# Performance work log

Hardware: AMD Instinct MI355X
Metric: run time of the kernel (lower is better)

## Reference

```python
import jax, jax.numpy as jnp
import numpy as np

NOPE, ROPE, VDIM, QKD = 128, 64, 128, 192
H = 16
EPS = 1e-6
SCALING = QKD ** -0.5


def rms_norm(x, w):
    xf = x.astype(jnp.float32)
    var = jnp.mean(xf * xf, axis=-1, keepdims=True)
    return (w * (xf * jax.lax.rsqrt(var + EPS))).astype(x.dtype)


def rotate_half(x):
    d = x.shape[-1] // 2
    return jnp.concatenate((-x[..., d:], x[..., :d]), axis=-1)


def apply_rope(q, k, cos, sin):
    # cos/sin: [B,S,D] -> unsqueeze head dim
    cos = cos[:, None, :, :]
    sin = sin[:, None, :, :]
    return q * cos + rotate_half(q) * sin, k * cos + rotate_half(k) * sin


def setup_inputs() -> dict:
    key = jax.random.key(0)
    ks = jax.random.split(key, 8)
    B, S, D = 2, 2048, 2048
    pos = jnp.arange(S, dtype=jnp.float32)
    inv_freq = 1.0 / (10000.0 ** (jnp.arange(0, ROPE, 2, dtype=jnp.float32) / ROPE))
    ang = pos[:, None] * inv_freq[None, :]            # [S, ROPE/2]
    emb = jnp.concatenate([ang, ang], axis=-1)        # [S, ROPE]
    cos = jnp.broadcast_to(jnp.cos(emb)[None], (B, S, ROPE))
    sin = jnp.broadcast_to(jnp.sin(emb)[None], (B, S, ROPE))
    s = lambda k, shp, fan: jax.random.normal(k, shp, jnp.float32) * (fan ** -0.5)
    return {
        "hidden_states": jax.random.normal(ks[0], (B, S, D), jnp.float32),
        "cos": cos,
        "sin": sin,
        "q_a_W": s(ks[1], (1536, D), D),
        "q_a_norm_w": jnp.ones((1536,), jnp.float32),
        "q_b_W": s(ks[2], (H * QKD, 1536), 1536),
        "kv_a_W": s(ks[3], (512 + ROPE, D), D),
        "kv_a_norm_w": jnp.ones((512,), jnp.float32),
        "kv_b_W": s(ks[4], (H * (NOPE + VDIM), 512), 512),
        "o_W": s(ks[5], (D, H * VDIM), H * VDIM),
    }


def reference(hidden_states, cos, sin, q_a_W, q_a_norm_w, q_b_W, kv_a_W,
              kv_a_norm_w, kv_b_W, o_W):
    B, S, D = hidden_states.shape
    # low-rank Q path
    q = rms_norm(hidden_states @ q_a_W.T, q_a_norm_w) @ q_b_W.T   # [B,S,H*QKD]
    q = q.reshape(B, S, H, QKD).transpose(0, 2, 1, 3)             # [B,H,S,QKD]
    q_pass, q_rot = q[..., :NOPE], q[..., NOPE:]
    # compressed KV path
    ckv = hidden_states @ kv_a_W.T                                # [B,S,512+ROPE]
    k_lat, k_rot = ckv[..., :512], ckv[..., 512:]
    kv = rms_norm(k_lat, kv_a_norm_w) @ kv_b_W.T                  # [B,S,H*(NOPE+VDIM)]
    kv = kv.reshape(B, S, H, NOPE + VDIM).transpose(0, 2, 1, 3)   # [B,H,S,*]
    k_pass, v = kv[..., :NOPE], kv[..., NOPE:]
    k_rot = k_rot.reshape(B, 1, S, ROPE)
    q_rot, k_rot = apply_rope(q_rot, k_rot, cos, sin)
    k_rot = jnp.broadcast_to(k_rot, (B, H, S, ROPE))
    query = jnp.concatenate((q_pass, q_rot), axis=-1)             # [B,H,S,QKD]
    key = jnp.concatenate((k_pass, k_rot), axis=-1)
    # eager causal attention
    scores = jnp.einsum('bhsd,bhtd->bhst', query, key) * SCALING
    causal = jnp.tril(jnp.ones((S, S), bool))
    scores = jnp.where(causal, scores, jnp.finfo(scores.dtype).min)
    attn = jax.nn.softmax(scores.astype(jnp.float32), axis=-1).astype(query.dtype)
    out = jnp.einsum('bhst,bhtd->bhsd', attn, v)                  # [B,H,S,VDIM]
    out = out.transpose(0, 2, 1, 3).reshape(B, S, H * VDIM)
    return out @ o_W.T
```

## Files before the change

### kernel.cpp

```cpp
#include <hip/hip_runtime.h>
#include <hip/hip_bf16.h>


typedef __bf16 bf16x8 __attribute__((ext_vector_type(8)));
typedef float floatx4 __attribute__((ext_vector_type(4)));
#define BF16 __hip_bfloat16

static __device__ __forceinline__ BF16 f2b(float x) { return __float2bfloat16(x); }
static __device__ __forceinline__ unsigned short b2u(BF16 x) { return *(unsigned short*)&x; }
static __device__ __forceinline__ float fast_exp2(float x) { return __builtin_amdgcn_exp2f(x); }

static __device__ __forceinline__ void load_lds16(const BF16* g, BF16* l) {
  __builtin_amdgcn_global_load_lds((__attribute__((address_space(1))) void*)(void*)g,
                                   (__attribute__((address_space(3))) void*)(void*)l,
                                   16, 0, 0);
}

struct CastArgs {
  const float* src[6];
  BF16* dst[6];
  long n[6];
};
__global__ void cast_multi_k(CastArgs a) {
  int r = blockIdx.y;
  long n = a.n[r];
  const float* __restrict__ x = a.src[r];
  BF16* __restrict__ y = a.dst[r];
  for (long i = ((long)blockIdx.x * 256 + threadIdx.x) * 4; i + 3 < n;
       i += (long)gridDim.x * 1024) {
    float4 v = *(const float4*)(x + i);
    y[i+0] = f2b(v.x); y[i+1] = f2b(v.y); y[i+2] = f2b(v.z); y[i+3] = f2b(v.w);
  }
}

template<int OUT_MODE>
__global__ __launch_bounds__(256) void gemm_lds(const BF16* __restrict__ A, const BF16* __restrict__ B,
                                                void* __restrict__ C, int M, int N, int K,
                                                const float* __restrict__ cosb,
                                                const float* __restrict__ sinb,
                                                BF16* __restrict__ P1, BF16* __restrict__ P2) {
  __shared__ __align__(16) BF16 As[128*32];
  __shared__ __align__(16) BF16 Bs[128*32];
  int tid = threadIdx.x, wave = tid >> 6, lane = tid & 63;
  int wr = wave >> 1, wc = wave & 1, lr = lane & 15, quad = lane >> 4;
  long m0 = (long)blockIdx.y * 128, n0 = (long)blockIdx.x * 128;

  int c0 = wave*64 + lane, c1 = c0 + 256;
  const BF16* ga0 = A + (m0 + (c0>>2))*(long)K + (c0&3)*8;
  const BF16* ga1 = A + (m0 + (c1>>2))*(long)K + (c1&3)*8;
  long bn0 = n0 + (c0>>2); if (bn0 >= N) bn0 = N-1;
  long bn1 = n0 + (c1>>2); if (bn1 >= N) bn1 = N-1;
  const BF16* gb0 = B + bn0*(long)K + (c0&3)*8;
  const BF16* gb1 = B + bn1*(long)K + (c1&3)*8;
  BF16* la0 = As + wave*512;
  BF16* la1 = As + wave*512 + 2048;
  BF16* lb0 = Bs + wave*512;
  BF16* lb1 = Bs + wave*512 + 2048;

  floatx4 acc[4][4] = {};
  for (int k0 = 0; k0 < K; k0 += 32) {
    __syncthreads();
    load_lds16(ga0 + k0, la0);
    load_lds16(ga1 + k0, la1);
    load_lds16(gb0 + k0, lb0);
    load_lds16(gb1 + k0, lb1);
    __syncthreads();
    bf16x8 a[4], b[4];
#pragma unroll
    for (int i = 0; i < 4; i++) a[i] = *(const bf16x8*)(As + (wr*64 + i*16 + lr)*32 + quad*8);
#pragma unroll
    for (int j = 0; j < 4; j++) b[j] = *(const bf16x8*)(Bs + (wc*64 + j*16 + lr)*32 + quad*8);
#pragma unroll
    for (int i = 0; i < 4; i++)
#pragma unroll
      for (int j = 0; j < 4; j++)
        acc[i][j] = __builtin_amdgcn_mfma_f32_16x16x32_bf16(a[i], b[j], acc[i][j], 0, 0, 0);
  }

  long n0w = n0 + wc*64;
  const float SCALE_L2E = 0.104117546f;
#pragma unroll
  for (int i = 0; i < 4; i++) {
    long tok = m0 + wr*64 + i*16 + quad*4;
    long bb = tok >> 11, s = tok & 2047;
    if (OUT_MODE == 0) {
#pragma unroll
      for (int r = 0; r < 4; r++) {
        long row = tok + r;
#pragma unroll
        for (int j = 0; j < 4; j++) {
          long col = n0w + j*16 + lr;
          if (col < N) ((float*)C)[row*(long)N + col] = acc[i][j][r];
        }
      }
    } else if (OUT_MODE == 2) {
#pragma unroll
      for (int j = 0; j < 4; j++) {
        long col = n0w + j*16 + lr;
        long h = col >> 8, d = col & 255;
        if (d < 128) {
#pragma unroll
          for (int r = 0; r < 4; r++)
            P1[((bb*16 + h)*2048 + s + r)*192 + d] = f2b(acc[i][j][r]);
        } else {
          ushort4 pk;
          pk.x = b2u(f2b(acc[i][j][0])); pk.y = b2u(f2b(acc[i][j][1]));
          pk.z = b2u(f2b(acc[i][j][2])); pk.w = b2u(f2b(acc[i][j][3]));
          *(ushort4*)(P2 + ((bb*16 + h)*128 + d - 128)*2048 + s) = pk;
        }
      }
    } else {
      bool rope = ((n0w % 192) == 128);
#pragma unroll
      for (int r = 0; r < 4; r++) {
        long row = tok + r;
#pragma unroll
        for (int j = 0; j < 4; j++) {
          long col = n0w + j*16 + lr;
          float x = acc[i][j][r], val;
          if (rope) {
            int id = j*16 + lr;
            float partner = acc[i][j^2][r];
            float rot = (j < 2) ? -partner : partner;
            val = x*cosb[row*64 + id] + rot*sinb[row*64 + id];
          } else {
            val = x;
          }
          long h = col / 192, d = col % 192;
          P1[((bb*16 + h)*2048 + s + r)*192 + d] = f2b(val * SCALE_L2E);
        }
      }
    }
  }
}

template<int D>
__global__ __launch_bounds__(256) void rmsnorm_k(const float* __restrict__ x, const float* __restrict__ w,
                                                 BF16* __restrict__ y, int ld_in, int ld_out) {
  long row = blockIdx.x;
  const float* xr = x + row * (long)ld_in;
  float ss = 0.f;
  for (int i = threadIdx.x * 4; i < D; i += 1024) {
    float4 v = *(const float4*)(xr + i);
    ss += v.x*v.x + v.y*v.y + v.z*v.z + v.w*v.w;
  }
#pragma unroll
  for (int off = 32; off > 0; off >>= 1) ss += __shfl_down(ss, off);
  __shared__ float red[4];
  if ((threadIdx.x & 63) == 0) red[threadIdx.x >> 6] = ss;
  __syncthreads();
  float tot = red[0] + red[1] + red[2] + red[3];
  float rs = rsqrtf(tot / (float)D + 1e-6f);
  BF16* yr = y + row * (long)ld_out;
  for (int i = threadIdx.x * 4; i < D; i += 1024) {
    float4 v = *(const float4*)(xr + i);
    yr[i+0] = f2b(v.x * w[i+0] * rs);
    yr[i+1] = f2b(v.y * w[i+1] * rs);
    yr[i+2] = f2b(v.z * w[i+2] * rs);
    yr[i+3] = f2b(v.w * w[i+3] * rs);
  }
}

__global__ void prep_krot_k(const float* __restrict__ krot, int ld, const float* __restrict__ cosb,
                            const float* __restrict__ sinb, BF16* __restrict__ Kt) {
  long row = blockIdx.x; int i = threadIdx.x;
  const float* kr = krot + row * (long)ld;
  float x = kr[i];
  float rot = (i < 32) ? -kr[i + 32] : kr[i - 32];
  BF16 v = f2b(x * cosb[row*64 + i] + rot * sinb[row*64 + i]);
  long b = row >> 11, s = row & 2047;
  long base = ((b*16)*2048 + s)*192 + 128 + i;
#pragma unroll
  for (int h = 0; h < 16; h++) Kt[base + (long)h*2048*192] = v;
}

#define LK 200
#define LV 72
#define LP 72
__global__ __launch_bounds__(256) void flash_k(const BF16* __restrict__ Qt, const BF16* __restrict__ Kt,
                                               const BF16* __restrict__ Vt, BF16* __restrict__ O) {
  __shared__ __align__(16) BF16 Ks[64*LK];
  __shared__ __align__(16) BF16 Vs[128*LV];
  __shared__ __align__(16) BF16 Ps[4][16*LP];
  int tid = threadIdx.x, wave = tid >> 6, lane = tid & 63;
  int lr = lane & 15, quad = lane >> 4;
  int F = blockIdx.x;
  int g = F & 31, jidx = F >> 5;
  int h = g & 15, b = g >> 4;
  const BF16* Qb = Qt + ((long)(b*16 + h) * 2048) * 192;
  const BF16* Kb = Kt + ((long)(b*16 + h) * 2048) * 192;
  const BF16* Vb = Vt + ((long)(b*16 + h) * 128) * 2048;
  const float NEG_INF = -__builtin_inff();

  int krow[6], kcol[6];
#pragma unroll
  for (int i = 0; i < 6; i++) {
    int c = tid + 256*i;
    krow[i] = c / 24; kcol[i] = (c % 24) * 8;
  }
  int vrow[4], vcol[4];
#pragma unroll
  for (int i = 0; i < 4; i++) {
    int c = tid + 256*i;
    vrow[i] = c >> 3; vcol[i] = (c & 7) * 8;
  }

  bf16x8 kreg[6], vreg[4];
  auto stage_load = [&](int k0) {
#pragma unroll
    for (int i = 0; i < 6; i++)
      kreg[i] = *(const bf16x8*)(Kb + (long)(k0 + krow[i])*192 + kcol[i]);
#pragma unroll
    for (int i = 0; i < 4; i++)
      vreg[i] = *(const bf16x8*)(Vb + (long)vrow[i]*2048 + k0 + vcol[i]);
  };
  auto stage_store = [&]() {
#pragma unroll
    for (int i = 0; i < 6; i++)
      *(bf16x8*)(Ks + krow[i]*LK + kcol[i]) = kreg[i];
#pragma unroll
    for (int i = 0; i < 4; i++)
      *(bf16x8*)(Vs + vrow[i]*LV + vcol[i]) = vreg[i];
  };

  for (int half = 0; half < 2; half++) {
    int qt = (half == 0) ? jidx : 31 - jidx;
    int q0 = qt * 64;
    bf16x8 qf[6];
    {
      const BF16* qp = Qb + (long)(q0 + wave*16 + lr) * 192 + quad*8;
#pragma unroll
      for (int f = 0; f < 6; f++) qf[f] = *(const bf16x8*)(qp + f*32);
    }
    float m_i[4], l_i[4];
#pragma unroll
    for (int r = 0; r < 4; r++) { m_i[r] = NEG_INF; l_i[r] = 0.f; }
    floatx4 o_acc[8] = {};
    int nk = qt + 1;
    stage_load(0);
    for (int kt = 0; kt < nk; kt++) {
      __syncthreads();
      stage_store();
      __syncthreads();
      if (kt + 1 < nk) stage_load((kt + 1) * 64);
      floatx4 st[4];
#pragma unroll
      for (int t = 0; t < 4; t++) {
        floatx4 c = {};
#pragma unroll
        for (int f = 0; f < 6; f++) {
          bf16x8 kf = *(const bf16x8*)(Ks + (t*16+lr)*LK + f*32 + quad*8);
          c = __builtin_amdgcn_mfma_f32_16x16x32_bf16(qf[f], kf, c, 0, 0, 0);
        }
        st[t] = c;
      }
      float mt[4];
#pragma unroll
      for (int r = 0; r < 4; r++) mt[r] = NEG_INF;
      if (kt == qt) {
#pragma unroll
        for (int t = 0; t < 4; t++) {
          int coff = t*16 + lr;
#pragma unroll
          for (int r = 0; r < 4; r++) {
            float sc = st[t][r];
            if (coff > wave*16 + quad*4 + r) sc = NEG_INF;
            st[t][r] = sc;
            mt[r] = fmaxf(mt[r], sc);
          }
        }
      } else {
#pragma unroll
        for (int t = 0; t < 4; t++)
#pragma unroll
          for (int r = 0; r < 4; r++) mt[r] = fmaxf(mt[r], st[t][r]);
      }
#pragma unroll
      for (int off = 1; off < 16; off <<= 1)
#pragma unroll
        for (int r = 0; r < 4; r++) mt[r] = fmaxf(mt[r], __shfl_xor(mt[r], off));
      float alpha[4], rsum[4];
#pragma unroll
      for (int r = 0; r < 4; r++) {
        float mn = fmaxf(m_i[r], mt[r]);
        alpha[r] = fast_exp2(m_i[r] - mn);
        m_i[r] = mn;
        rsum[r] = 0.f;
      }
#pragma unroll
      for (int t = 0; t < 4; t++)
#pragma unroll
        for (int r = 0; r < 4; r++) {
          float p = fast_exp2(st[t][r] - m_i[r]);
          st[t][r] = p;
          rsum[r] += p;
        }
#pragma unroll
      for (int off = 1; off < 16; off <<= 1)
#pragma unroll
        for (int r = 0; r < 4; r++) rsum[r] += __shfl_xor(rsum[r], off);
#pragma unroll
      for (int r = 0; r < 4; r++) l_i[r] = l_i[r]*alpha[r] + rsum[r];
#pragma unroll
      for (int v = 0; v < 8; v++)
#pragma unroll
        for (int r = 0; r < 4; r++) o_acc[v][r] *= alpha[r];
#pragma unroll
      for (int t = 0; t < 4; t++)
#pragma unroll
        for (int r = 0; r < 4; r++)
          Ps[wave][(quad*4 + r)*LP + t*16 + lr] = f2b(st[t][r]);
#pragma unroll
      for (int kc = 0; kc < 2; kc++) {
        bf16x8 pa = *(const bf16x8*)(&Ps[wave][lr*LP + kc*32 + quad*8]);
#pragma unroll
        for (int v = 0; v < 8; v++) {
          bf16x8 vf = *(const bf16x8*)(&Vs[(v*16+lr)*LV + kc*32 + quad*8]);
          o_acc[v] = __builtin_amdgcn_mfma_f32_16x16x32_bf16(pa, vf, o_acc[v], 0, 0, 0);
        }
      }
    }
    long rowb = q0 + wave*16 + quad*4;
#pragma unroll
    for (int v = 0; v < 8; v++)
#pragma unroll
      for (int r = 0; r < 4; r++) {
        long row = rowb + r;
        O[((long)b*2048 + row)*2048 + h*128 + v*16 + lr] = f2b(o_acc[v][r] / l_i[r]);
      }
  }
}

extern "C" void kernel_launch(void* const* d_in, const int* in_sizes, int n_in,
                              void* d_out, int out_size, void* d_ws, size_t ws_size,
                              hipStream_t stream) {
  const float* hidden      = (const float*)d_in[0];
  const float* cosb        = (const float*)d_in[1];
  const float* sinb        = (const float*)d_in[2];
  const float* q_a_W       = (const float*)d_in[3];
  const float* q_a_norm_w  = (const float*)d_in[4];
  const float* q_b_W       = (const float*)d_in[5];
  const float* kv_a_W      = (const float*)d_in[6];
  const float* kv_a_norm_w = (const float*)d_in[7];
  const float* kv_b_W      = (const float*)d_in[8];
  const float* o_W         = (const float*)d_in[9];
  float* out = (float*)d_out;

  const int Mrows = 4096;

  char* ws = (char*)d_ws; size_t off = 0;
  auto alloc = [&](size_t bytes) -> void* {
    void* p = ws + off; off = (off + bytes + 255) & ~(size_t)255; return p;
  };
  BF16* hb    = (BF16*)alloc((size_t)4096*2048*2);
  BF16* Wqakv = (BF16*)alloc((size_t)2112*2048*2);
  BF16* Wqb   = (BF16*)alloc((size_t)3072*1536*2);
  BF16* Wkvb  = (BF16*)alloc((size_t)4096*512*2);
  BF16* Wo    = (BF16*)alloc((size_t)2048*2048*2);
  float* qakv = (float*)alloc((size_t)4096*2112*4);
  BF16* qan   = (BF16*)alloc((size_t)4096*1536*2);
  BF16* kvn   = (BF16*)alloc((size_t)4096*512*2);
  BF16* Qt    = (BF16*)alloc((size_t)2*16*2048*192*2);
  BF16* Kt    = (BF16*)alloc((size_t)2*16*2048*192*2);
  BF16* Vt    = (BF16*)alloc((size_t)2*16*128*2048*2);
  BF16* attn  = (BF16*)alloc((size_t)4096*2048*2);

  CastArgs ca;
  ca.src[0] = hidden;  ca.dst[0] = hb;                 ca.n[0] = (long)4096*2048;
  ca.src[1] = q_a_W;   ca.dst[1] = Wqakv;              ca.n[1] = (long)1536*2048;
  ca.src[2] = kv_a_W;  ca.dst[2] = Wqakv + (long)1536*2048; ca.n[2] = (long)576*2048;
  ca.src[3] = q_b_W;   ca.dst[3] = Wqb;                ca.n[3] = (long)3072*1536;
  ca.src[4] = kv_b_W;  ca.dst[4] = Wkvb;               ca.n[4] = (long)4096*512;
  ca.src[5] = o_W;     ca.dst[5] = Wo;                 ca.n[5] = (long)2048*2048;
  cast_multi_k<<<dim3(1024, 6), dim3(256), 0, stream>>>(ca);

  gemm_lds<0><<<dim3(17, 32), dim3(256), 0, stream>>>(hb, Wqakv, qakv, Mrows, 2112, 2048,
                                                      nullptr, nullptr, nullptr, nullptr);
  rmsnorm_k<1536><<<dim3(4096), dim3(256), 0, stream>>>(qakv, q_a_norm_w, qan, 2112, 1536);
  rmsnorm_k<512><<<dim3(4096), dim3(256), 0, stream>>>(qakv + 1536, kv_a_norm_w, kvn, 2112, 512);
  prep_krot_k<<<dim3(4096), dim3(64), 0, stream>>>(qakv + 2048, 2112, cosb, sinb, Kt);

  gemm_lds<3><<<dim3(24, 32), dim3(256), 0, stream>>>(qan, Wqb, nullptr, Mrows, 3072, 1536,
                                                      cosb, sinb, Qt, nullptr);
  gemm_lds<2><<<dim3(32, 32), dim3(256), 0, stream>>>(kvn, Wkvb, nullptr, Mrows, 4096, 512,
                                                      nullptr, nullptr, Kt, Vt);

  flash_k<<<dim3(512), dim3(256), 0, stream>>>(Qt, Kt, Vt, attn);

  gemm_lds<0><<<dim3(16, 32), dim3(256), 0, stream>>>(attn, Wo, out, Mrows, 2048, 2048,
                                                      nullptr, nullptr, nullptr, nullptr);
}
```

Before: 490.4 us.

## Merge norm/rope kernels, batch Q and KV GEMMs, widen flash tiles

The two RMSNorm launches and the k_rot RoPE kernel become one per-row kernel. The Q-projection and KV-projection GEMMs run as a single launch split by block index. The flash attention kernel now uses 512-thread blocks over 128-row query tiles, so each K/V tile loaded into LDS is shared by 8 waves, with per-wave causal skipping. This cuts launch count and K/V global traffic, at the cost of half as many flash blocks and possible wave idling on diagonal tiles.

Measured after the change: 492.5 us. No clear change (+0.4%).

```diff
diff --git a/kernel.cpp b/kernel.cpp
--- a/kernel.cpp
+++ b/kernel.cpp
@@ -34,16 +34,13 @@
 }
 
 template<int OUT_MODE>
-__global__ __launch_bounds__(256) void gemm_lds(const BF16* __restrict__ A, const BF16* __restrict__ B,
-                                                void* __restrict__ C, int M, int N, int K,
-                                                const float* __restrict__ cosb,
-                                                const float* __restrict__ sinb,
-                                                BF16* __restrict__ P1, BF16* __restrict__ P2) {
-  __shared__ __align__(16) BF16 As[128*32];
-  __shared__ __align__(16) BF16 Bs[128*32];
+static __device__ __forceinline__ void gemm_body(
+    const BF16* __restrict__ A, const BF16* __restrict__ B, void* __restrict__ C,
+    int M, int N, int K, const float* __restrict__ cosb, const float* __restrict__ sinb,
+    BF16* __restrict__ P1, BF16* __restrict__ P2, int bx, int by, BF16* As, BF16* Bs) {
   int tid = threadIdx.x, wave = tid >> 6, lane = tid & 63;
   int wr = wave >> 1, wc = wave & 1, lr = lane & 15, quad = lane >> 4;
-  long m0 = (long)blockIdx.y * 128, n0 = (long)blockIdx.x * 128;
+  long m0 = (long)by * 128, n0 = (long)bx * 128;
 
   int c0 = wave*64 + lane, c1 = c0 + 256;
   const BF16* ga0 = A + (m0 + (c0>>2))*(long)K + (c0&3)*8;
@@ -134,101 +131,151 @@
   }
 }
 
-template<int D>
-__global__ __launch_bounds__(256) void rmsnorm_k(const float* __restrict__ x, const float* __restrict__ w,
-                                                 BF16* __restrict__ y, int ld_in, int ld_out) {
+__global__ __launch_bounds__(256) void gemm0_k(const BF16* __restrict__ A, const BF16* __restrict__ B,
+                                               float* __restrict__ C, int M, int N, int K) {
+  __shared__ __align__(16) BF16 As[128*32];
+  __shared__ __align__(16) BF16 Bs[128*32];
+  gemm_body<0>(A, B, C, M, N, K, nullptr, nullptr, nullptr, nullptr,
+               blockIdx.x, blockIdx.y, As, Bs);
+}
+
+__global__ __launch_bounds__(256) void gemm_qkv_k(const BF16* __restrict__ qan, const BF16* __restrict__ Wqb,
+                                                  const BF16* __restrict__ kvn, const BF16* __restrict__ Wkvb,
+                                                  const float* __restrict__ cosb, const float* __restrict__ sinb,
+                                                  BF16* __restrict__ Qt, BF16* __restrict__ Kt,
+                                                  BF16* __restrict__ Vt) {
+  __shared__ __align__(16) BF16 As[128*32];
+  __shared__ __align__(16) BF16 Bs[128*32];
+  int bid = blockIdx.x;
+  if (bid < 768) {
+    gemm_body<3>(qan, Wqb, nullptr, 4096, 3072, 1536, cosb, sinb, Qt, nullptr,
+                 bid % 24, bid / 24, As, Bs);
+  } else {
+    bid -= 768;
+    gemm_body<2>(kvn, Wkvb, nullptr, 4096, 4096, 512, nullptr, nullptr, Kt, Vt,
+                 bid % 32, bid / 32, As, Bs);
+  }
+}
+
+__global__ __launch_bounds__(256) void norms_k(const float* __restrict__ qakv,
+                                               const float* __restrict__ qw, const float* __restrict__ kw,
+                                               const float* __restrict__ cosb, const float* __restrict__ sinb,
+                                               BF16* __restrict__ qan, BF16* __restrict__ kvn,
+                                               BF16* __restrict__ Kt) {
   long row = blockIdx.x;
-  const float* xr = x + row * (long)ld_in;
-  float ss = 0.f;
-  for (int i = threadIdx.x * 4; i < D; i += 1024) {
-    float4 v = *(const float4*)(xr + i);
-    ss += v.x*v.x + v.y*v.y + v.z*v.z + v.w*v.w;
-  }
-#pragma unroll
-  for (int off = 32; off > 0; off >>= 1) ss += __shfl_down(ss, off);
+  const float* xr = qakv + row * 2112;
+  int tid = threadIdx.x;
   __shared__ float red[4];
-  if ((threadIdx.x & 63) == 0) red[threadIdx.x >> 6] = ss;
+  {
+    float ss = 0.f;
+    for (int i = tid*4; i < 1536; i += 1024) {
+      float4 v = *(const float4*)(xr + i);
+      ss += v.x*v.x + v.y*v.y + v.z*v.z + v.w*v.w;
+    }
+#pragma unroll
+    for (int off = 32; off > 0; off >>= 1) ss += __shfl_down(ss, off);
+    if ((tid & 63) == 0) red[tid >> 6] = ss;
+    __syncthreads();
+    float rs = rsqrtf((red[0]+red[1]+red[2]+red[3]) / 1536.f + 1e-6f);
+    BF16* yr = qan + row * 1536;
+    for (int i = tid*4; i < 1536; i += 1024) {
+      float4 v = *(const float4*)(xr + i);
+      yr[i+0] = f2b(v.x * qw[i+0] * rs);
+      yr[i+1] = f2b(v.y * qw[i+1] * rs);
+      yr[i+2] = f2b(v.z * qw[i+2] * rs);
+      yr[i+3] = f2b(v.w * qw[i+3] * rs);
+    }
+  }
   __syncthreads();
-  float tot = red[0] + red[1] + red[2] + red[3];
-  float rs = rsqrtf(tot / (float)D + 1e-6f);
-  BF16* yr = y + row * (long)ld_out;
-  for (int i = threadIdx.x * 4; i < D; i += 1024) {
-    float4 v = *(const float4*)(xr + i);
-    yr[i+0] = f2b(v.x * w[i+0] * rs);
-    yr[i+1] = f2b(v.y * w[i+1] * rs);
-    yr[i+2] = f2b(v.z * w[i+2] * rs);
-    yr[i+3] = f2b(v.w * w[i+3] * rs);
-  }
-}
-
-__global__ void prep_krot_k(const float* __restrict__ krot, int ld, const float* __restrict__ cosb,
-                            const float* __restrict__ sinb, BF16* __restrict__ Kt) {
-  long row = blockIdx.x; int i = threadIdx.x;
-  const float* kr = krot + row * (long)ld;
-  float x = kr[i];
-  float rot = (i < 32) ? -kr[i + 32] : kr[i - 32];
-  BF16 v = f2b(x * cosb[row*64 + i] + rot * sinb[row*64 + i]);
-  long b = row >> 11, s = row & 2047;
-  long base = ((b*16)*2048 + s)*192 + 128 + i;
-#pragma unroll
-  for (int h = 0; h < 16; h++) Kt[base + (long)h*2048*192] = v;
+  {
+    float ss = 0.f;
+    for (int i = tid*4; i < 512; i += 1024) {
+      float4 v = *(const float4*)(xr + 1536 + i);
+      ss += v.x*v.x + v.y*v.y + v.z*v.z + v.w*v.w;
+    }
+#pragma unroll
+    for (int off = 32; off > 0; off >>= 1) ss += __shfl_down(ss, off);
+    if ((tid & 63) == 0) red[tid >> 6] = ss;
+    __syncthreads();
+    float rs = rsqrtf((red[0]+red[1]+red[2]+red[3]) / 512.f + 1e-6f);
+    BF16* yr = kvn + row * 512;
+    for (int i = tid*4; i < 512; i += 1024) {
+      float4 v = *(const float4*)(xr + 1536 + i);
+      yr[i+0] = f2b(v.x * kw[i+0] * rs);
+      yr[i+1] = f2b(v.y * kw[i+1] * rs);
+      yr[i+2] = f2b(v.z * kw[i+2] * rs);
+      yr[i+3] = f2b(v.w * kw[i+3] * rs);
+    }
+  }
+  if (tid < 64) {
+    int i = tid;
+    const float* kr = xr + 2048;
+    float x = kr[i];
+    float rot = (i < 32) ? -kr[i + 32] : kr[i - 32];
+    BF16 v = f2b(x * cosb[row*64 + i] + rot * sinb[row*64 + i]);
+    long b = row >> 11, s = row & 2047;
+    long base = ((b*16)*2048 + s)*192 + 128 + i;
+#pragma unroll
+    for (int h = 0; h < 16; h++) Kt[base + (long)h*2048*192] = v;
+  }
 }
 
 #define LK 200
 #define LV 72
 #define LP 72
-__global__ __launch_bounds__(256) void flash_k(const BF16* __restrict__ Qt, const BF16* __restrict__ Kt,
+__global__ __launch_bounds__(512) void flash_k(const BF16* __restrict__ Qt, const BF16* __restrict__ Kt,
                                                const BF16* __restrict__ Vt, BF16* __restrict__ O) {
   __shared__ __align__(16) BF16 Ks[64*LK];
   __shared__ __align__(16) BF16 Vs[128*LV];
-  __shared__ __align__(16) BF16 Ps[4][16*LP];
+  __shared__ __align__(16) BF16 Ps[8][16*LP];
   int tid = threadIdx.x, wave = tid >> 6, lane = tid & 63;
   int lr = lane & 15, quad = lane >> 4;
   int F = blockIdx.x;
-  int g = F & 31, jidx = F >> 5;
+  int g = F & 31, j = F >> 5;
   int h = g & 15, b = g >> 4;
   const BF16* Qb = Qt + ((long)(b*16 + h) * 2048) * 192;
   const BF16* Kb = Kt + ((long)(b*16 + h) * 2048) * 192;
   const BF16* Vb = Vt + ((long)(b*16 + h) * 128) * 2048;
   const float NEG_INF = -__builtin_inff();
 
-  int krow[6], kcol[6];
-#pragma unroll
-  for (int i = 0; i < 6; i++) {
-    int c = tid + 256*i;
+  int krow[3], kcol[3];
+#pragma unroll
+  for (int i = 0; i < 3; i++) {
+    int c = tid + 512*i;
     krow[i] = c / 24; kcol[i] = (c % 24) * 8;
   }
-  int vrow[4], vcol[4];
-#pragma unroll
-  for (int i = 0; i < 4; i++) {
-    int c = tid + 256*i;
+  int vrow[2], vcol[2];
+#pragma unroll
+  for (int i = 0; i < 2; i++) {
+    int c = tid + 512*i;
     vrow[i] = c >> 3; vcol[i] = (c & 7) * 8;
   }
 
-  bf16x8 kreg[6], vreg[4];
+  bf16x8 kreg[3], vreg[2];
   auto stage_load = [&](int k0) {
 #pragma unroll
-    for (int i = 0; i < 6; i++)
+    for (int i = 0; i < 3; i++)
       kreg[i] = *(const bf16x8*)(Kb + (long)(k0 + krow[i])*192 + kcol[i]);
 #pragma unroll
-    for (int i = 0; i < 4; i++)
+    for (int i = 0; i < 2; i++)
       vreg[i] = *(const bf16x8*)(Vb + (long)vrow[i]*2048 + k0 + vcol[i]);
   };
   auto stage_store = [&]() {
 #pragma unroll
-    for (int i = 0; i < 6; i++)
+    for (int i = 0; i < 3; i++)
       *(bf16x8*)(Ks + krow[i]*LK + kcol[i]) = kreg[i];
 #pragma unroll
-    for (int i = 0; i < 4; i++)
+    for (int i = 0; i < 2; i++)
       *(bf16x8*)(Vs + vrow[i]*LV + vcol[i]) = vreg[i];
   };
 
   for (int half = 0; half < 2; half++) {
-    int qt = (half == 0) ? jidx : 31 - jidx;
-    int q0 = qt * 64;
+    int qt = (half == 0) ? j : 15 - j;
+    int q0 = qt * 128;
+    int wq0 = q0 + wave*16;
     bf16x8 qf[6];
     {
-      const BF16* qp = Qb + (long)(q0 + wave*16 + lr) * 192 + quad*8;
+      const BF16* qp = Qb + (long)(wq0 + lr) * 192 + quad*8;
 #pragma unroll
       for (int f = 0; f < 6; f++) qf[f] = *(const bf16x8*)(qp + f*32);
     }
@@ -236,13 +283,14 @@
 #pragma unroll
     for (int r = 0; r < 4; r++) { m_i[r] = NEG_INF; l_i[r] = 0.f; }
     floatx4 o_acc[8] = {};
-    int nk = qt + 1;
+    int nk = 2*qt + 2;
     stage_load(0);
     for (int kt = 0; kt < nk; kt++) {
       __syncthreads();
       stage_store();
       __syncthreads();
       if (kt + 1 < nk) stage_load((kt + 1) * 64);
+      if (kt*64 > wq0 + 15) continue;
       floatx4 st[4];
 #pragma unroll
       for (int t = 0; t < 4; t++) {
@@ -257,14 +305,15 @@
       float mt[4];
 #pragma unroll
       for (int r = 0; r < 4; r++) mt[r] = NEG_INF;
-      if (kt == qt) {
+      if (kt*64 + 63 > wq0) {
+        int rbase = wq0 + quad*4 - kt*64;
 #pragma unroll
         for (int t = 0; t < 4; t++) {
           int coff = t*16 + lr;
 #pragma unroll
           for (int r = 0; r < 4; r++) {
             float sc = st[t][r];
-            if (coff > wave*16 + quad*4 + r) sc = NEG_INF;
+            if (coff > rbase + r) sc = NEG_INF;
             st[t][r] = sc;
             mt[r] = fmaxf(mt[r], sc);
           }
@@ -320,7 +369,7 @@
         }
       }
     }
-    long rowb = q0 + wave*16 + quad*4;
+    long rowb = wq0 + quad*4;
 #pragma unroll
     for (int v = 0; v < 8; v++)
 #pragma unroll
@@ -374,19 +423,14 @@
   ca.src[5] = o_W;     ca.dst[5] = Wo;                 ca.n[5] = (long)2048*2048;
   cast_multi_k<<<dim3(1024, 6), dim3(256), 0, stream>>>(ca);
 
-  gemm_lds<0><<<dim3(17, 32), dim3(256), 0, stream>>>(hb, Wqakv, qakv, Mrows, 2112, 2048,
-                                                      nullptr, nullptr, nullptr, nullptr);
-  rmsnorm_k<1536><<<dim3(4096), dim3(256), 0, stream>>>(qakv, q_a_norm_w, qan, 2112, 1536);
-  rmsnorm_k<512><<<dim3(4096), dim3(256), 0, stream>>>(qakv + 1536, kv_a_norm_w, kvn, 2112, 512);
-  prep_krot_k<<<dim3(4096), dim3(64), 0, stream>>>(qakv + 2048, 2112, cosb, sinb, Kt);
-
-  gemm_lds<3><<<dim3(24, 32), dim3(256), 0, stream>>>(qan, Wqb, nullptr, Mrows, 3072, 1536,
-                                                      cosb, sinb, Qt, nullptr);
-  gemm_lds<2><<<dim3(32, 32), dim3(256), 0, stream>>>(kvn, Wkvb, nullptr, Mrows, 4096, 512,
-                                                      nullptr, nullptr, Kt, Vt);
-
-  flash_k<<<dim3(512), dim3(256), 0, stream>>>(Qt, Kt, Vt, attn);
-
-  gemm_lds<0><<<dim3(16, 32), dim3(256), 0, stream>>>(attn, Wo, out, Mrows, 2048, 2048,
-                                                      nullptr, nullptr, nullptr, nullptr);
-}
+  gemm0_k<<<dim3(17, 32), dim3(256), 0, stream>>>(hb, Wqakv, qakv, Mrows, 2112, 2048);
+
+  norms_k<<<dim3(4096), dim3(256), 0, stream>>>(qakv, q_a_norm_w, kv_a_norm_w,
+                                                cosb, sinb, qan, kvn, Kt);
+
+  gemm_qkv_k<<<dim3(1792), dim3(256), 0, stream>>>(qan, Wqb, kvn, Wkvb, cosb, sinb, Qt, Kt, Vt);
+
+  flash_k<<<dim3(256), dim3(512), 0, stream>>>(Qt, Kt, Vt, attn);
+
+  gemm0_k<<<dim3(16, 32), dim3(256), 0, stream>>>(attn, Wo, out, Mrows, 2048, 2048);
+}
```
